# Performance work log

Measured on AMD Instinct MI355X. Metric: run time of the kernel, lower is better.

The kernel has to match this reference:

```python
import jax, jax.numpy as jnp
import numpy as np

B, T, S, D, H, DK, DV = 4, 2048, 2048, 1024, 16, 64, 64


def setup_inputs() -> dict:
    key = jax.random.key(0)
    ks = jax.random.split(key, 12)
    sq = 1.0 / np.sqrt(D)
    return {
        "query": jax.random.normal(ks[0], (B, T, D), jnp.float32),
        "value": jax.random.normal(ks[1], (B, S, D), jnp.float32),
        "mask": jnp.ones((B, T, S), dtype=bool),
        "Wq": jax.random.normal(ks[2], (D, H, DK), jnp.float32) * sq,
        "bq": jnp.zeros((H, DK), jnp.float32),
        "Wk": jax.random.normal(ks[3], (D, H, DK), jnp.float32) * sq,
        "bk": jnp.zeros((H, DK), jnp.float32),
        "Wv": jax.random.normal(ks[4], (D, H, DV), jnp.float32) * sq,
        "bv": jnp.zeros((H, DV), jnp.float32),
        "Wo": jax.random.normal(ks[5], (H, DV, D), jnp.float32) * (1.0 / np.sqrt(H * DV)),
        "bo": jnp.zeros((D,), jnp.float32),
    }


def reference(query, value, mask, Wq, bq, Wk, bk, Wv, bv, Wo, bo):
    # key input defaults to value when only [query, value] is given
    q = jnp.einsum("btd,dhk->bthk", query, Wq) + bq  # [B,T,H,DK]
    k = jnp.einsum("bsd,dhk->bshk", value, Wk) + bk  # [B,S,H,DK]
    v = jnp.einsum("bsd,dhv->bshv", value, Wv) + bv  # [B,S,H,DV]
    # dot_product_equation 'aecd,abcd->acbe': scores[b,h,t,s]
    scores = jnp.einsum("bshk,bthk->bhts", k, q) * (1.0 / np.sqrt(DK))
    # MaskedSoftmax: mask [B,T,S] expanded at axis 1 -> [B,1,T,S]
    adder = (1.0 - mask[:, None, :, :].astype(scores.dtype)) * -10000.0
    probs = jax.nn.softmax(scores + adder, axis=-1)
    # combine_equation 'acbe,aecd->abcd'
    attn = jnp.einsum("bhts,bshv->bthv", probs, v)  # [B,T,H,DV]
    out = jnp.einsum("bthv,hvd->btd", attn, Wo) + bo  # [B,T,D]
    return out
```

## Files before the change

kernel.cpp:

```cpp
#include <hip/hip_runtime.h>

typedef __bf16 bf16x8 __attribute__((ext_vector_type(8)));
typedef __bf16 bf16x4 __attribute__((ext_vector_type(4)));
typedef float  f32x4  __attribute__((ext_vector_type(4)));
typedef int    i32x4  __attribute__((ext_vector_type(4)));

typedef __attribute__((address_space(1))) unsigned int as1_u32;
typedef __attribute__((address_space(3))) unsigned int as3_u32;

#define DEVI __device__ __forceinline__

DEVI unsigned short f2bf(float f) {
    union { float f; unsigned u; } v; v.f = f;
    unsigned r = (v.u + 0x7fffu + ((v.u >> 16) & 1u)) >> 16;
    return (unsigned short)r;
}

DEVI void gload16(const void* g, void* l) {
    __builtin_amdgcn_global_load_lds((const as1_u32*)g, (as3_u32*)l, 16, 0, 0);
}

#define C_EXP 0.18033688011112042f
#define MASK_ADD (-14426.950408889634f)

__global__ __launch_bounds__(256) void cvt2_kernel(const float* __restrict__ in0,
                                                   unsigned short* __restrict__ out0,
                                                   const float* __restrict__ in1,
                                                   unsigned short* __restrict__ out1,
                                                   int n8) {
    const int stride = gridDim.x * 256;
    const int total = 2 * n8;
    for (int idx = blockIdx.x * 256 + threadIdx.x; idx < total; idx += stride) {
        const int sel = idx >= n8;
        const int j = sel ? idx - n8 : idx;
        const float* in = sel ? in1 : in0;
        unsigned short* out = sel ? out1 : out0;
        const f32x4 a = *(const f32x4*)(in + (size_t)j * 8);
        const f32x4 b = *(const f32x4*)(in + (size_t)j * 8 + 4);
        union { bf16x4 v[2]; i32x4 q; } u;
        u.v[0] = __builtin_convertvector(a, bf16x4);
        u.v[1] = __builtin_convertvector(b, bf16x4);
        *(i32x4*)(out + (size_t)j * 8) = u.q;
    }
}

__global__ __launch_bounds__(256) void wtrans_kernel(const float* __restrict__ W0,
                                                     const float* __restrict__ W1,
                                                     const float* __restrict__ W2,
                                                     const float* __restrict__ W3,
                                                     unsigned short* __restrict__ T0,
                                                     unsigned short* __restrict__ T1,
                                                     unsigned short* __restrict__ T2,
                                                     unsigned short* __restrict__ T3) {
    __shared__ float tile[64][65];
    const float* W;
    unsigned short* WT;
    float scale = 1.0f;
    switch (blockIdx.z) {
        case 0:  W = W0; WT = T0; scale = C_EXP; break;
        case 1:  W = W1; WT = T1; break;
        case 2:  W = W2; WT = T2; break;
        default: W = W3; WT = T3; break;
    }
    const int k0 = blockIdx.x * 64, n0 = blockIdx.y * 64;
    const int i = threadIdx.x;
    const int c4 = (i & 15) * 4, rbase = i >> 4;
    for (int rr = 0; rr < 4; ++rr) {
        const int kl = rbase + rr * 16;
        const float4 v = *(const float4*)(W + (size_t)(k0 + kl) * 1024 + n0 + c4);
        tile[kl][c4 + 0] = v.x; tile[kl][c4 + 1] = v.y;
        tile[kl][c4 + 2] = v.z; tile[kl][c4 + 3] = v.w;
    }
    __syncthreads();
    for (int rr = 0; rr < 4; ++rr) {
        const int nl = rbase + rr * 16;
        ushort4 o;
        o.x = f2bf(tile[c4 + 0][nl] * scale); o.y = f2bf(tile[c4 + 1][nl] * scale);
        o.z = f2bf(tile[c4 + 2][nl] * scale); o.w = f2bf(tile[c4 + 3][nl] * scale);
        *(ushort4*)(WT + (size_t)(n0 + nl) * 1024 + k0 + c4) = o;
    }
}

__global__ __launch_bounds__(256) void maskflag_kernel(const int* __restrict__ mask,
                                                       unsigned* __restrict__ flagsW) {
    const int bid = blockIdx.x;
    const int b = bid >> 9, rem = bid & 511;
    const int tb = rem >> 5, si = rem & 31;
    const int i = threadIdx.x;
    const int t = tb * 128 + (i >> 1);
    const int s = si * 64 + (i & 1) * 32;
    const uint4* p = (const uint4*)(mask + ((size_t)(b * 2048 + t)) * 2048 + s);
    int ok = 1;
    #pragma unroll
    for (int u = 0; u < 8; ++u) {
        const uint4 a = p[u];
        ok &= (a.x != 0) & (a.y != 0) & (a.z != 0) & (a.w != 0);
    }
    int all = __syncthreads_and(ok);
    if (i == 0 && !all) atomicOr(&flagsW[b * 16 + tb], 1u << si);
}

template <int MODE, int NB>
__global__ __launch_bounds__(256) void mm_kernel(const unsigned short* __restrict__ A,
                                                 const unsigned short* __restrict__ BT,
                                                 const float* __restrict__ biasK,
                                                 const float* __restrict__ biasV,
                                                 float bscale,
                                                 void* __restrict__ OvK,
                                                 void* __restrict__ OvV) {
    __shared__ __align__(16) unsigned short Ab[2][128 * 64];
    __shared__ __align__(16) unsigned short Bb[2][128 * 64];
    const int bid = blockIdx.x;
    const int xcd = bid & 7, jj = bid >> 3;
    const int n0 = (jj % NB) * 128;
    const int m0 = ((jj / NB) * 8 + xcd) * 128;
    const int i = threadIdx.x, w = i >> 6, l = i & 63;
    const int wm = w >> 1, wn = w & 1;
    const int c = l & 15, g = l >> 4;
    const int srow = l >> 3, sslot = l & 7;

    f32x4 acc[4][4] = {};

    const unsigned short* As[4];
    const unsigned short* Bs[4];
    unsigned lofs[4];
    #pragma unroll
    for (int u = 0; u < 4; ++u) {
        const int rl = w * 32 + u * 8 + srow;
        const int ch = sslot ^ ((rl ^ (rl >> 2)) & 7);
        As[u] = A  + (size_t)(m0 + rl) * 1024 + ch * 8;
        Bs[u] = BT + (size_t)(n0 + rl) * 1024 + ch * 8;
        lofs[u] = (unsigned)((w * 32 + u * 8) * 64);
    }

    #pragma unroll
    for (int u = 0; u < 4; ++u) {
        gload16(As[u], &Ab[0][lofs[u]]);
        gload16(Bs[u], &Bb[0][lofs[u]]);
    }
    __syncthreads();

    int rsA[4], rsB[4];
    #pragma unroll
    for (int f = 0; f < 4; ++f) {
        const int ra = wm * 64 + f * 16 + c;
        const int rb = wn * 64 + f * 16 + c;
        rsA[f] = (ra ^ (ra >> 2)) & 7;
        rsB[f] = (rb ^ (rb >> 2)) & 7;
    }

    #pragma unroll 2
    for (int it = 0; it < 16; ++it) {
        const int buf = it & 1;
        if (it < 15) {
            #pragma unroll
            for (int u = 0; u < 4; ++u) {
                gload16(As[u] + (it + 1) * 64, &Ab[buf ^ 1][lofs[u]]);
                gload16(Bs[u] + (it + 1) * 64, &Bb[buf ^ 1][lofs[u]]);
            }
        }
        bf16x8 af[4][2], bfr[4][2];
        #pragma unroll
        for (int f = 0; f < 4; ++f)
            #pragma unroll
            for (int kk = 0; kk < 2; ++kk) {
                af[f][kk]  = *(const bf16x8*)&Ab[buf][(wm * 64 + f * 16 + c) * 64 + (((kk * 4 + g) ^ rsA[f]) * 8)];
                bfr[f][kk] = *(const bf16x8*)&Bb[buf][(wn * 64 + f * 16 + c) * 64 + (((kk * 4 + g) ^ rsB[f]) * 8)];
            }
        __builtin_amdgcn_s_setprio(1);
        #pragma unroll
        for (int kk = 0; kk < 2; ++kk)
            #pragma unroll
            for (int mf = 0; mf < 4; ++mf)
                #pragma unroll
                for (int nf = 0; nf < 4; ++nf)
                    acc[mf][nf] = __builtin_amdgcn_mfma_f32_16x16x32_bf16(af[mf][kk], bfr[nf][kk], acc[mf][nf], 0, 0, 0);
        __builtin_amdgcn_s_setprio(0);
        __syncthreads();
    }

    #pragma unroll
    for (int nf = 0; nf < 4; ++nf) {
        const int n = n0 + wn * 64 + nf * 16 + c;
        if (MODE == 0 || (MODE == 3 && n0 < 1024)) {
            const float bv = biasK[n] * bscale;
            const int h = n >> 6, cc = n & 63;
            unsigned short* O = (unsigned short*)OvK;
            #pragma unroll
            for (int mf = 0; mf < 4; ++mf) {
                const int mbase = m0 + wm * 64 + mf * 16 + g * 4;
                const int b = mbase >> 11, t = mbase & 2047;
                #pragma unroll
                for (int r = 0; r < 4; ++r)
                    O[(((size_t)(b * 16 + h)) * 2048 + t + r) * 64 + cc] = f2bf(acc[mf][nf][r] + bv);
            }
        } else if (MODE == 3) {
            const int nn = n - 1024;
            const float bv = biasV[nn];
            const int h = nn >> 6, cc = nn & 63;
            unsigned short* O = (unsigned short*)OvV;
            #pragma unroll
            for (int mf = 0; mf < 4; ++mf) {
                const int mbase = m0 + wm * 64 + mf * 16 + g * 4;
                const int b = mbase >> 11, t = mbase & 2047;
                f32x4 v;
                #pragma unroll
                for (int r = 0; r < 4; ++r) v[r] = acc[mf][nf][r] + bv;
                bf16x4 pv = __builtin_convertvector(v, bf16x4);
                *(bf16x4*)(O + (((size_t)(b * 16 + h)) * 64 + cc) * 2048 + t) = pv;
            }
        } else {
            const float bv = biasK[n] * bscale;
            float* O = (float*)OvK;
            #pragma unroll
            for (int mf = 0; mf < 4; ++mf) {
                const int mbase = m0 + wm * 64 + mf * 16 + g * 4;
                #pragma unroll
                for (int r = 0; r < 4; ++r)
                    O[(size_t)(mbase + r) * 1024 + n] = acc[mf][nf][r] + bv;
            }
        }
    }
}

__global__ __launch_bounds__(256, 4) void attn_kernel(const unsigned short* __restrict__ Qp,
                                                      const unsigned short* __restrict__ Kp,
                                                      const unsigned short* __restrict__ VTp,
                                                      const int* __restrict__ mask,
                                                      const unsigned* __restrict__ flagsW,
                                                      unsigned short* __restrict__ attnb) {
    __shared__ __align__(16) unsigned short Kt[2][64 * 64];
    __shared__ __align__(16) unsigned short Vt[2][64 * 64];

    const int bid = blockIdx.x;
    const int xcd = bid & 7, jj = bid >> 3;
    const int bh = xcd * 8 + (jj >> 4);
    const int tb = jj & 15;
    const int b = bh >> 4, h = bh & 15;
    const int i = threadIdx.x, w = i >> 6, l = i & 63;
    const int c = l & 15, g = l >> 4;

    const unsigned short* Qb  = Qp  + (size_t)bh * 2048 * 64;
    const unsigned short* Kb  = Kp  + (size_t)bh * 2048 * 64;
    const unsigned short* VTb = VTp + (size_t)bh * 64 * 2048;

    const int twave = tb * 128 + w * 32;
    const int tA = twave + c, tB = twave + 16 + c;

    const unsigned notall = __builtin_amdgcn_readfirstlane(flagsW[b * 16 + tb]);

    bf16x8 qfA[2], qfB[2];
    #pragma unroll
    for (int kq = 0; kq < 2; ++kq) {
        qfA[kq] = *(const bf16x8*)(Qb + (size_t)tA * 64 + kq * 32 + g * 8);
        qfB[kq] = *(const bf16x8*)(Qb + (size_t)tB * 64 + kq * 32 + g * 8);
    }

    f32x4 oA[4] = {}, oB[4] = {};
    f32x4 daccA = {}, daccB = {};
    const f32x4 zf = {};

    bf16x8 ones8;
    #pragma unroll
    for (int j = 0; j < 8; ++j) ones8[j] = (__bf16)1.0f;

    int rrow[4], rswz[4];
    #pragma unroll
    for (int sm = 0; sm < 4; ++sm) {
        rrow[sm] = (sm >> 1) * 32 + (c >> 2) * 8 + (sm & 1) * 4 + (c & 3);
        rswz[sm] = (rrow[sm] ^ (rrow[sm] >> 2)) & 7;
    }
    int vswz[4];
    #pragma unroll
    for (int vm = 0; vm < 4; ++vm) {
        const int rv = vm * 16 + c;
        vswz[vm] = (rv ^ (rv >> 2)) & 7;
    }

    const int srow = l >> 3, sslot = l & 7;

    const unsigned short* kstage[2];
    const unsigned short* vstage[2];
    #pragma unroll
    for (int u = 0; u < 2; ++u) {
        const int row = w * 16 + u * 8 + srow;
        const int ch = sslot ^ ((row ^ (row >> 2)) & 7);
        gload16(Kb + (size_t)row * 64 + ch * 8, &Kt[0][(w * 16 + u * 8) * 64]);
        gload16(VTb + (size_t)row * 2048 + ch * 8, &Vt[0][(w * 16 + u * 8) * 64]);
        kstage[u] = Kb + (size_t)(64 + row) * 64 + ch * 8;
        vstage[u] = VTb + (size_t)row * 2048 + 64 + ch * 8;
    }
    __syncthreads();

    #pragma unroll 2
    for (int it = 0; it < 32; ++it) {
        const int buf = it & 1;
        const int s0 = it * 64;

        if (it < 31) {
            #pragma unroll
            for (int u = 0; u < 2; ++u) {
                gload16(kstage[u], &Kt[buf ^ 1][(w * 16 + u * 8) * 64]);
                gload16(vstage[u], &Vt[buf ^ 1][(w * 16 + u * 8) * 64]);
                kstage[u] += 64 * 64;
                vstage[u] += 64;
            }
        }

        f32x4 scA[4], scB[4];
        __builtin_amdgcn_s_setprio(1);
        #pragma unroll
        for (int sm = 0; sm < 4; ++sm) {
            #pragma unroll
            for (int kq = 0; kq < 2; ++kq) {
                const bf16x8 kf = *(const bf16x8*)&Kt[buf][rrow[sm] * 64 + (((kq * 4 + g) ^ rswz[sm]) * 8)];
                if (kq == 0) {
                    scA[sm] = __builtin_amdgcn_mfma_f32_16x16x32_bf16(kf, qfA[0], zf, 0, 0, 0);
                    scB[sm] = __builtin_amdgcn_mfma_f32_16x16x32_bf16(kf, qfB[0], zf, 0, 0, 0);
                } else {
                    scA[sm] = __builtin_amdgcn_mfma_f32_16x16x32_bf16(kf, qfA[1], scA[sm], 0, 0, 0);
                    scB[sm] = __builtin_amdgcn_mfma_f32_16x16x32_bf16(kf, qfB[1], scB[sm], 0, 0, 0);
                }
            }
        }
        __builtin_amdgcn_s_setprio(0);

        if (notall & (1u << it)) {
            #pragma unroll
            for (int sm = 0; sm < 4; ++sm)
                #pragma unroll
                for (int r = 0; r < 4; ++r) {
                    const int s = s0 + (sm >> 1) * 32 + g * 8 + (sm & 1) * 4 + r;
                    if (mask[(size_t)(b * 2048 + tA) * 2048 + s] == 0) scA[sm][r] += MASK_ADD;
                    if (mask[(size_t)(b * 2048 + tB) * 2048 + s] == 0) scB[sm][r] += MASK_ADD;
                }
        }

        bf16x8 paA[2], paB[2];
        #pragma unroll
        for (int kv = 0; kv < 2; ++kv) {
            f32x4 a0, a1, b0, b1;
            #pragma unroll
            for (int r = 0; r < 4; ++r) {
                a0[r] = __builtin_amdgcn_exp2f(scA[kv * 2][r]);
                a1[r] = __builtin_amdgcn_exp2f(scA[kv * 2 + 1][r]);
                b0[r] = __builtin_amdgcn_exp2f(scB[kv * 2][r]);
                b1[r] = __builtin_amdgcn_exp2f(scB[kv * 2 + 1][r]);
            }
            union { struct { bf16x4 lo, hi; } hh; bf16x8 v; } ua, ub;
            ua.hh.lo = __builtin_convertvector(a0, bf16x4);
            ua.hh.hi = __builtin_convertvector(a1, bf16x4);
            ub.hh.lo = __builtin_convertvector(b0, bf16x4);
            ub.hh.hi = __builtin_convertvector(b1, bf16x4);
            paA[kv] = ua.v;
            paB[kv] = ub.v;
        }

        __builtin_amdgcn_s_setprio(1);
        #pragma unroll
        for (int kv = 0; kv < 2; ++kv) {
            daccA = __builtin_amdgcn_mfma_f32_16x16x32_bf16(ones8, paA[kv], daccA, 0, 0, 0);
            daccB = __builtin_amdgcn_mfma_f32_16x16x32_bf16(ones8, paB[kv], daccB, 0, 0, 0);
            #pragma unroll
            for (int vm = 0; vm < 4; ++vm) {
                const bf16x8 vf = *(const bf16x8*)&Vt[buf][(vm * 16 + c) * 64 + (((kv * 4 + g) ^ vswz[vm]) * 8)];
                oA[vm] = __builtin_amdgcn_mfma_f32_16x16x32_bf16(vf, paA[kv], oA[vm], 0, 0, 0);
                oB[vm] = __builtin_amdgcn_mfma_f32_16x16x32_bf16(vf, paB[kv], oB[vm], 0, 0, 0);
            }
        }
        __builtin_amdgcn_s_setprio(0);

        __syncthreads();
    }

    const float invA = 1.0f / daccA[0];
    const float invB = 1.0f / daccB[0];

    #pragma unroll
    for (int vm = 0; vm < 4; ++vm) {
        f32x4 vA, vB;
        #pragma unroll
        for (int r = 0; r < 4; ++r) { vA[r] = oA[vm][r] * invA; vB[r] = oB[vm][r] * invB; }
        bf16x4 pA = __builtin_convertvector(vA, bf16x4);
        bf16x4 pB = __builtin_convertvector(vB, bf16x4);
        *(bf16x4*)(attnb + (size_t)(b * 2048 + tA) * 1024 + h * 64 + vm * 16 + g * 4) = pA;
        *(bf16x4*)(attnb + (size_t)(b * 2048 + tB) * 1024 + h * 64 + vm * 16 + g * 4) = pB;
    }
}

extern "C" void kernel_launch(void* const* d_in, const int* in_sizes, int n_in,
                              void* d_out, int out_size, void* d_ws, size_t ws_size,
                              hipStream_t stream) {
    const float* query = (const float*)d_in[0];
    const float* value = (const float*)d_in[1];
    const int*   mask  = (const int*)d_in[2];
    const float* Wq = (const float*)d_in[3];
    const float* bq = (const float*)d_in[4];
    const float* Wk = (const float*)d_in[5];
    const float* bk = (const float*)d_in[6];
    const float* Wv = (const float*)d_in[7];
    const float* bv = (const float*)d_in[8];
    const float* Wo = (const float*)d_in[9];
    const float* bo = (const float*)d_in[10];

    char* ws = (char*)d_ws;
    unsigned short* WqT   = (unsigned short*)(ws + ((size_t)0  << 20));
    unsigned short* WkT   = (unsigned short*)(ws + ((size_t)2  << 20));
    unsigned short* WvT   = (unsigned short*)(ws + ((size_t)4  << 20));
    unsigned short* WoT   = (unsigned short*)(ws + ((size_t)6  << 20));
    unsigned*       flagsW= (unsigned*)      (ws + ((size_t)8  << 20));
    unsigned short* VCONV = (unsigned short*)(ws + ((size_t)9  << 20));
    unsigned short* QCONV = (unsigned short*)(ws + ((size_t)25 << 20));
    unsigned short* Kp    = (unsigned short*)(ws + ((size_t)41 << 20));
    unsigned short* VTp   = (unsigned short*)(ws + ((size_t)57 << 20));
    unsigned short* Qp    = VCONV;
    unsigned short* attnb = QCONV;

    const int n8 = 8192 * 1024 / 8;

    hipMemsetAsync(flagsW, 0, 64 * sizeof(unsigned), stream);

    cvt2_kernel<<<2048, 256, 0, stream>>>(value, VCONV, query, QCONV, n8);
    wtrans_kernel<<<dim3(16, 16, 4), 256, 0, stream>>>(Wq, Wk, Wv, Wo, WqT, WkT, WvT, WoT);
    maskflag_kernel<<<2048, 256, 0, stream>>>(mask, flagsW);

    mm_kernel<3, 16><<<1024, 256, 0, stream>>>(VCONV, WkT, bk, bv, 1.0f, Kp, VTp);
    mm_kernel<0, 8><<<512, 256, 0, stream>>>(QCONV, WqT, bq, bq, C_EXP, Qp, nullptr);

    attn_kernel<<<1024, 256, 0, stream>>>(Qp, Kp, VTp, mask, flagsW, attnb);

    mm_kernel<2, 8><<<512, 256, 0, stream>>>(attnb, WoT, bo, bo, 1.0f, d_out, nullptr);
}
```

Before: 202.2 us.

## Merge prepass kernels and fuse Q/K/V projections into one GEMM launch

After: 192.3 us (median of 2 runs). 4.9% less time.

```diff
diff --git a/kernel.cpp b/kernel.cpp
--- a/kernel.cpp
+++ b/kernel.cpp
@@ -23,91 +23,96 @@
 #define C_EXP 0.18033688011112042f
 #define MASK_ADD (-14426.950408889634f)
 
-__global__ __launch_bounds__(256) void cvt2_kernel(const float* __restrict__ in0,
-                                                   unsigned short* __restrict__ out0,
-                                                   const float* __restrict__ in1,
-                                                   unsigned short* __restrict__ out1,
-                                                   int n8) {
-    const int stride = gridDim.x * 256;
-    const int total = 2 * n8;
-    for (int idx = blockIdx.x * 256 + threadIdx.x; idx < total; idx += stride) {
-        const int sel = idx >= n8;
-        const int j = sel ? idx - n8 : idx;
-        const float* in = sel ? in1 : in0;
-        unsigned short* out = sel ? out1 : out0;
-        const f32x4 a = *(const f32x4*)(in + (size_t)j * 8);
-        const f32x4 b = *(const f32x4*)(in + (size_t)j * 8 + 4);
-        union { bf16x4 v[2]; i32x4 q; } u;
-        u.v[0] = __builtin_convertvector(a, bf16x4);
-        u.v[1] = __builtin_convertvector(b, bf16x4);
-        *(i32x4*)(out + (size_t)j * 8) = u.q;
-    }
-}
-
-__global__ __launch_bounds__(256) void wtrans_kernel(const float* __restrict__ W0,
-                                                     const float* __restrict__ W1,
-                                                     const float* __restrict__ W2,
-                                                     const float* __restrict__ W3,
-                                                     unsigned short* __restrict__ T0,
-                                                     unsigned short* __restrict__ T1,
-                                                     unsigned short* __restrict__ T2,
-                                                     unsigned short* __restrict__ T3) {
+__global__ __launch_bounds__(256) void prepass_kernel(const float* __restrict__ value,
+                                                      unsigned short* __restrict__ VCONV,
+                                                      const float* __restrict__ query,
+                                                      unsigned short* __restrict__ QCONV,
+                                                      const float* __restrict__ Wq,
+                                                      const float* __restrict__ Wk,
+                                                      const float* __restrict__ Wv,
+                                                      const float* __restrict__ Wo,
+                                                      unsigned short* __restrict__ WqT,
+                                                      unsigned short* __restrict__ WkT,
+                                                      unsigned short* __restrict__ WvT,
+                                                      unsigned short* __restrict__ WoT,
+                                                      const int* __restrict__ mask,
+                                                      unsigned char* __restrict__ flagsB) {
     __shared__ float tile[64][65];
-    const float* W;
-    unsigned short* WT;
-    float scale = 1.0f;
-    switch (blockIdx.z) {
-        case 0:  W = W0; WT = T0; scale = C_EXP; break;
-        case 1:  W = W1; WT = T1; break;
-        case 2:  W = W2; WT = T2; break;
-        default: W = W3; WT = T3; break;
-    }
-    const int k0 = blockIdx.x * 64, n0 = blockIdx.y * 64;
-    const int i = threadIdx.x;
-    const int c4 = (i & 15) * 4, rbase = i >> 4;
-    for (int rr = 0; rr < 4; ++rr) {
-        const int kl = rbase + rr * 16;
-        const float4 v = *(const float4*)(W + (size_t)(k0 + kl) * 1024 + n0 + c4);
-        tile[kl][c4 + 0] = v.x; tile[kl][c4 + 1] = v.y;
-        tile[kl][c4 + 2] = v.z; tile[kl][c4 + 3] = v.w;
-    }
-    __syncthreads();
-    for (int rr = 0; rr < 4; ++rr) {
-        const int nl = rbase + rr * 16;
-        ushort4 o;
-        o.x = f2bf(tile[c4 + 0][nl] * scale); o.y = f2bf(tile[c4 + 1][nl] * scale);
-        o.z = f2bf(tile[c4 + 2][nl] * scale); o.w = f2bf(tile[c4 + 3][nl] * scale);
-        *(ushort4*)(WT + (size_t)(n0 + nl) * 1024 + k0 + c4) = o;
-    }
-}
-
-__global__ __launch_bounds__(256) void maskflag_kernel(const int* __restrict__ mask,
-                                                       unsigned* __restrict__ flagsW) {
     const int bid = blockIdx.x;
-    const int b = bid >> 9, rem = bid & 511;
-    const int tb = rem >> 5, si = rem & 31;
-    const int i = threadIdx.x;
-    const int t = tb * 128 + (i >> 1);
-    const int s = si * 64 + (i & 1) * 32;
-    const uint4* p = (const uint4*)(mask + ((size_t)(b * 2048 + t)) * 2048 + s);
-    int ok = 1;
-    #pragma unroll
-    for (int u = 0; u < 8; ++u) {
-        const uint4 a = p[u];
-        ok &= (a.x != 0) & (a.y != 0) & (a.z != 0) & (a.w != 0);
-    }
-    int all = __syncthreads_and(ok);
-    if (i == 0 && !all) atomicOr(&flagsW[b * 16 + tb], 1u << si);
+    const int tid = threadIdx.x;
+
+    if (bid < 2048) {
+        const int n8 = 8192 * 1024 / 8;
+        const int total = 2 * n8;
+        for (int idx = bid * 256 + tid; idx < total; idx += 2048 * 256) {
+            const int sel = idx >= n8;
+            const int j = sel ? idx - n8 : idx;
+            const float* in = sel ? query : value;
+            unsigned short* out = sel ? QCONV : VCONV;
+            const f32x4 a = *(const f32x4*)(in + (size_t)j * 8);
+            const f32x4 b = *(const f32x4*)(in + (size_t)j * 8 + 4);
+            union { bf16x4 v[2]; i32x4 q; } u;
+            u.v[0] = __builtin_convertvector(a, bf16x4);
+            u.v[1] = __builtin_convertvector(b, bf16x4);
+            *(i32x4*)(out + (size_t)j * 8) = u.q;
+        }
+    } else if (bid < 3072) {
+        const int e = bid - 2048;
+        const int bx = e & 15, by = (e >> 4) & 15, z = e >> 8;
+        const float* W;
+        unsigned short* WT;
+        float scale = 1.0f;
+        switch (z) {
+            case 0:  W = Wq; WT = WqT; scale = C_EXP; break;
+            case 1:  W = Wk; WT = WkT; break;
+            case 2:  W = Wv; WT = WvT; break;
+            default: W = Wo; WT = WoT; break;
+        }
+        const int k0 = bx * 64, n0 = by * 64;
+        const int c4 = (tid & 15) * 4, rbase = tid >> 4;
+        for (int rr = 0; rr < 4; ++rr) {
+            const int kl = rbase + rr * 16;
+            const float4 v = *(const float4*)(W + (size_t)(k0 + kl) * 1024 + n0 + c4);
+            tile[kl][c4 + 0] = v.x; tile[kl][c4 + 1] = v.y;
+            tile[kl][c4 + 2] = v.z; tile[kl][c4 + 3] = v.w;
+        }
+        __syncthreads();
+        for (int rr = 0; rr < 4; ++rr) {
+            const int nl = rbase + rr * 16;
+            ushort4 o;
+            o.x = f2bf(tile[c4 + 0][nl] * scale); o.y = f2bf(tile[c4 + 1][nl] * scale);
+            o.z = f2bf(tile[c4 + 2][nl] * scale); o.w = f2bf(tile[c4 + 3][nl] * scale);
+            *(ushort4*)(WT + (size_t)(n0 + nl) * 1024 + k0 + c4) = o;
+        }
+    } else {
+        const int e = bid - 3072;
+        const int b = e >> 9, rem = e & 511;
+        const int tb = rem >> 5, si = rem & 31;
+        const int t = tb * 128 + (tid >> 1);
+        const int s = si * 64 + (tid & 1) * 32;
+        const uint4* p = (const uint4*)(mask + ((size_t)(b * 2048 + t)) * 2048 + s);
+        int ok = 1;
+        #pragma unroll
+        for (int u = 0; u < 8; ++u) {
+            const uint4 a = p[u];
+            ok &= (a.x != 0) & (a.y != 0) & (a.z != 0) & (a.w != 0);
+        }
+        int all = __syncthreads_and(ok);
+        if (tid == 0) flagsB[(b * 16 + tb) * 32 + si] = (unsigned char)(!all);
+    }
 }
 
 template <int MODE, int NB>
-__global__ __launch_bounds__(256) void mm_kernel(const unsigned short* __restrict__ A,
+__global__ __launch_bounds__(256) void mm_kernel(const unsigned short* __restrict__ A0,
+                                                 const unsigned short* __restrict__ A1,
                                                  const unsigned short* __restrict__ BT,
                                                  const float* __restrict__ biasK,
                                                  const float* __restrict__ biasV,
+                                                 const float* __restrict__ biasQ,
                                                  float bscale,
                                                  void* __restrict__ OvK,
-                                                 void* __restrict__ OvV) {
+                                                 void* __restrict__ OvV,
+                                                 void* __restrict__ OvQ) {
     __shared__ __align__(16) unsigned short Ab[2][128 * 64];
     __shared__ __align__(16) unsigned short Bb[2][128 * 64];
     const int bid = blockIdx.x;
@@ -119,6 +124,8 @@
     const int c = l & 15, g = l >> 4;
     const int srow = l >> 3, sslot = l & 7;
 
+    const unsigned short* A = (MODE == 4 && n0 >= 2048) ? A1 : A0;
+
     f32x4 acc[4][4] = {};
 
     const unsigned short* As[4];
@@ -182,7 +189,10 @@
     #pragma unroll
     for (int nf = 0; nf < 4; ++nf) {
         const int n = n0 + wn * 64 + nf * 16 + c;
-        if (MODE == 0 || (MODE == 3 && n0 < 1024)) {
+        const bool isK = (MODE == 0) || ((MODE == 3 || MODE == 4) && n0 < 1024);
+        const bool isV = (MODE == 3 || MODE == 4) && n0 >= 1024 && n0 < 2048;
+        const bool isQ = (MODE == 4) && n0 >= 2048;
+        if (isK) {
             const float bv = biasK[n] * bscale;
             const int h = n >> 6, cc = n & 63;
             unsigned short* O = (unsigned short*)OvK;
@@ -194,7 +204,7 @@
                 for (int r = 0; r < 4; ++r)
                     O[(((size_t)(b * 16 + h)) * 2048 + t + r) * 64 + cc] = f2bf(acc[mf][nf][r] + bv);
             }
-        } else if (MODE == 3) {
+        } else if (isV) {
             const int nn = n - 1024;
             const float bv = biasV[nn];
             const int h = nn >> 6, cc = nn & 63;
@@ -209,6 +219,19 @@
                 bf16x4 pv = __builtin_convertvector(v, bf16x4);
                 *(bf16x4*)(O + (((size_t)(b * 16 + h)) * 64 + cc) * 2048 + t) = pv;
             }
+        } else if (isQ) {
+            const int nn = n - 2048;
+            const float bv = biasQ[nn] * C_EXP;
+            const int h = nn >> 6, cc = nn & 63;
+            unsigned short* O = (unsigned short*)OvQ;
+            #pragma unroll
+            for (int mf = 0; mf < 4; ++mf) {
+                const int mbase = m0 + wm * 64 + mf * 16 + g * 4;
+                const int b = mbase >> 11, t = mbase & 2047;
+                #pragma unroll
+                for (int r = 0; r < 4; ++r)
+                    O[(((size_t)(b * 16 + h)) * 2048 + t + r) * 64 + cc] = f2bf(acc[mf][nf][r] + bv);
+            }
         } else {
             const float bv = biasK[n] * bscale;
             float* O = (float*)OvK;
@@ -227,7 +250,7 @@
                                                       const unsigned short* __restrict__ Kp,
                                                       const unsigned short* __restrict__ VTp,
                                                       const int* __restrict__ mask,
-                                                      const unsigned* __restrict__ flagsW,
+                                                      const unsigned char* __restrict__ flagsB,
                                                       unsigned short* __restrict__ attnb) {
     __shared__ __align__(16) unsigned short Kt[2][64 * 64];
     __shared__ __align__(16) unsigned short Vt[2][64 * 64];
@@ -247,7 +270,8 @@
     const int twave = tb * 128 + w * 32;
     const int tA = twave + c, tB = twave + 16 + c;
 
-    const unsigned notall = __builtin_amdgcn_readfirstlane(flagsW[b * 16 + tb]);
+    const unsigned char myb = flagsB[(size_t)(b * 16 + tb) * 32 + (l & 31)];
+    const unsigned notall = (unsigned)__ballot(myb != 0);
 
     bf16x8 qfA[2], qfB[2];
     #pragma unroll
@@ -404,30 +428,36 @@
     const float* bo = (const float*)d_in[10];
 
     char* ws = (char*)d_ws;
-    unsigned short* WqT   = (unsigned short*)(ws + ((size_t)0  << 20));
-    unsigned short* WkT   = (unsigned short*)(ws + ((size_t)2  << 20));
-    unsigned short* WvT   = (unsigned short*)(ws + ((size_t)4  << 20));
+    unsigned short* WkT   = (unsigned short*)(ws + ((size_t)0  << 20));
+    unsigned short* WvT   = (unsigned short*)(ws + ((size_t)2  << 20));
+    unsigned short* WqT   = (unsigned short*)(ws + ((size_t)4  << 20));
     unsigned short* WoT   = (unsigned short*)(ws + ((size_t)6  << 20));
-    unsigned*       flagsW= (unsigned*)      (ws + ((size_t)8  << 20));
+    unsigned char*  flagsB= (unsigned char*) (ws + ((size_t)8  << 20));
     unsigned short* VCONV = (unsigned short*)(ws + ((size_t)9  << 20));
     unsigned short* QCONV = (unsigned short*)(ws + ((size_t)25 << 20));
     unsigned short* Kp    = (unsigned short*)(ws + ((size_t)41 << 20));
     unsigned short* VTp   = (unsigned short*)(ws + ((size_t)57 << 20));
-    unsigned short* Qp    = VCONV;
+
+    const bool merged = ws_size >= ((size_t)90 << 20);
+    unsigned short* Qp    = merged ? (unsigned short*)(ws + ((size_t)73 << 20)) : VCONV;
     unsigned short* attnb = QCONV;
 
-    const int n8 = 8192 * 1024 / 8;
-
-    hipMemsetAsync(flagsW, 0, 64 * sizeof(unsigned), stream);
-
-    cvt2_kernel<<<2048, 256, 0, stream>>>(value, VCONV, query, QCONV, n8);
-    wtrans_kernel<<<dim3(16, 16, 4), 256, 0, stream>>>(Wq, Wk, Wv, Wo, WqT, WkT, WvT, WoT);
-    maskflag_kernel<<<2048, 256, 0, stream>>>(mask, flagsW);
-
-    mm_kernel<3, 16><<<1024, 256, 0, stream>>>(VCONV, WkT, bk, bv, 1.0f, Kp, VTp);
-    mm_kernel<0, 8><<<512, 256, 0, stream>>>(QCONV, WqT, bq, bq, C_EXP, Qp, nullptr);
-
-    attn_kernel<<<1024, 256, 0, stream>>>(Qp, Kp, VTp, mask, flagsW, attnb);
-
-    mm_kernel<2, 8><<<512, 256, 0, stream>>>(attnb, WoT, bo, bo, 1.0f, d_out, nullptr);
-}
+    prepass_kernel<<<5120, 256, 0, stream>>>(value, VCONV, query, QCONV,
+                                             Wq, Wk, Wv, Wo, WqT, WkT, WvT, WoT,
+                                             mask, flagsB);
+
+    if (merged) {
+        mm_kernel<4, 24><<<1536, 256, 0, stream>>>(VCONV, QCONV, WkT, bk, bv, bq,
+                                                   1.0f, Kp, VTp, Qp);
+    } else {
+        mm_kernel<3, 16><<<1024, 256, 0, stream>>>(VCONV, nullptr, WkT, bk, bv, bq,
+                                                   1.0f, Kp, VTp, nullptr);
+        mm_kernel<0, 8><<<512, 256, 0, stream>>>(QCONV, nullptr, WqT, bq, bq, bq,
+                                                 C_EXP, Qp, nullptr, nullptr);
+    }
+
+    attn_kernel<<<1024, 256, 0, stream>>>(Qp, Kp, VTp, mask, flagsB, attnb);
+
+    mm_kernel<2, 8><<<512, 256, 0, stream>>>(attnb, nullptr, WoT, bo, bo, bo,
+                                             1.0f, d_out, nullptr, nullptr);
+}
```
